# Kernel optimization log

Hardware: AMD Instinct MI355X
Metric: run time of the kernel (lower is better)

## Reference

```python
import jax, jax.numpy as jnp
import numpy as np
from functools import partial

STRIDE = 32
NUM_CLASSES = 20
CONF_THRESH = 0.01
NMS_THRESH = 0.5
H = W = 96
C = 512


def setup_inputs() -> dict:
    key = jax.random.key(0)
    ks = jax.random.split(key, 6)
    cls_feat = jax.random.normal(ks[0], (1, C, H, W), dtype=jnp.float32)
    reg_feat = jax.random.normal(ks[1], (1, C, H, W), dtype=jnp.float32)
    # small init scale so sigmoid/exp stay in a realistic range
    obj_w = jax.random.normal(ks[2], (1, C), dtype=jnp.float32) * 0.05
    cls_w = jax.random.normal(ks[3], (NUM_CLASSES, C), dtype=jnp.float32) * 0.05
    reg_w = jax.random.normal(ks[4], (4, C), dtype=jnp.float32) * 0.05
    obj_b = jnp.zeros((1,), jnp.float32)
    cls_b = jnp.zeros((NUM_CLASSES,), jnp.float32)
    reg_b = jnp.zeros((4,), jnp.float32)
    return {"cls_feat": cls_feat, "reg_feat": reg_feat,
            "obj_w": obj_w, "obj_b": obj_b,
            "cls_w": cls_w, "cls_b": cls_b,
            "reg_w": reg_w, "reg_b": reg_b}


def _decode_and_score(cls_feat, reg_feat, obj_w, obj_b, cls_w, cls_b, reg_w, reg_b):
    # 1x1 convs == per-pixel matmul; permute(0,2,3,1).flatten(1,2), take batch 0
    _, _, h, w = cls_feat.shape
    obj = jnp.einsum('bchw,oc->bhwo', cls_feat, obj_w)[0].reshape(h * w, 1) + obj_b
    cls = jnp.einsum('bchw,oc->bhwo', cls_feat, cls_w)[0].reshape(h * w, NUM_CLASSES) + cls_b
    reg = jnp.einsum('bchw,oc->bhwo', reg_feat, reg_w)[0].reshape(h * w, 4) + reg_b
    scores_all = jax.nn.sigmoid(obj) * jax.nn.sigmoid(cls)            # [N, 20]
    # decode_boxes: grid of (x, y) cell coords, stride 32
    gy, gx = jnp.meshgrid(jnp.arange(h), jnp.arange(w), indexing='ij')
    grid = jnp.stack([gx, gy], axis=-1).reshape(-1, 2).astype(jnp.float32)
    ctr = (jax.nn.sigmoid(reg[:, :2]) + grid) * STRIDE               # [N, 2]
    wh = jnp.exp(reg[:, 2:]) * STRIDE                                # [N, 2]
    bboxes = jnp.concatenate([ctr - 0.5 * wh, ctr + 0.5 * wh], axis=-1)  # x1y1x2y2
    return bboxes, scores_all


@jax.jit
def reference(cls_feat, reg_feat, obj_w, obj_b, cls_w, cls_b, reg_w, reg_b):
    bboxes, scores_all = _decode_and_score(
        cls_feat, reg_feat, obj_w, obj_b, cls_w, cls_b, reg_w, reg_b)
    n = bboxes.shape[0]
    labels = jnp.argmax(scores_all, axis=1)                          # [N]
    scores = jnp.max(scores_all, axis=1)                             # [N]
    valid = scores >= CONF_THRESH
    # sort by score descending (invalid boxes pushed last)
    order = jnp.argsort(-jnp.where(valid, scores, -jnp.inf))
    b = bboxes[order]
    lab_s = labels[order]
    valid_s = valid[order]
    x1, y1, x2, y2 = b[:, 0], b[:, 1], b[:, 2], b[:, 3]
    areas = (x2 - x1) * (y2 - y1)
    # pairwise IoU, matching the numpy nms (1e-10 clamp on w/h)
    iw = jnp.maximum(1e-10, jnp.minimum(x2[:, None], x2[None, :]) - jnp.maximum(x1[:, None], x1[None, :]))
    ih = jnp.maximum(1e-10, jnp.minimum(y2[:, None], y2[None, :]) - jnp.maximum(y1[:, None], y1[None, :]))
    inter = iw * ih
    iou = inter / (areas[:, None] + areas[None, :] - inter)
    same_cls = lab_s[:, None] == lab_s[None, :]
    supp = (iou > NMS_THRESH) & same_cls                             # [N, N] suppression graph
    idx = jnp.arange(n)
    # greedy per-class NMS in score order: box i is kept iff no earlier
    # kept box of the same class has IoU > thresh with it
    def body(i, keep):
        suppressed = jnp.any(keep & supp[:, i] & (idx < i))
        return keep.at[i].set(valid_s[i] & ~suppressed)
    keep_s = jax.lax.fori_loop(0, n, body, jnp.zeros(n, dtype=bool))
    keep = jnp.zeros(n, dtype=bool).at[order].set(keep_s)            # unsort
    return bboxes, scores, labels, keep


if __name__ == '__main__':
    out = reference(**setup_inputs())
    print([o.shape for o in out], int(out[3].sum()))
```

## Files before the change

kernel.cpp:

```cpp
#include <hip/hip_runtime.h>

#define HW 9216
#define WIDTH 96
#define NCLS 20
#define NOUT 25
#define CAP 1024
#define NW 16

#define WS_KEYS   256
#define WS_PART   164096
#define WS_MASK   7536896

__global__ __launch_bounds__(256) void gemm_stage1(
    const float* __restrict__ cls_feat, const float* __restrict__ reg_feat,
    const float* __restrict__ obj_w, const float* __restrict__ cls_w,
    const float* __restrict__ reg_w, float* __restrict__ partial,
    unsigned* __restrict__ cnt)
{
    if (blockIdx.x == 0 && threadIdx.x < 64) cnt[threadIdx.x] = 0u;

    __shared__ float wlds[64 * 28];
    const int g   = blockIdx.x & 7;
    const int pos = (blockIdx.x >> 3) * 256 + threadIdx.x;
    const int cb  = g * 64;

    for (int i = threadIdx.x; i < 64 * 25; i += 256) {
        const int o = i >> 6, k = i & 63;
        float v;
        if (o == 0)        v = obj_w[cb + k];
        else if (o < 21)   v = cls_w[(o - 1) * 512 + cb + k];
        else               v = reg_w[(o - 21) * 512 + cb + k];
        wlds[k * 28 + o] = v;
    }
    __syncthreads();

    float acc[NOUT];
#pragma unroll
    for (int o = 0; o < NOUT; ++o) acc[o] = 0.f;

    const float* cf = cls_feat + (size_t)cb * HW + pos;
    const float* rf = reg_feat + (size_t)cb * HW + pos;

#pragma unroll 8
    for (int k = 0; k < 64; ++k) {
        float f = cf[(size_t)k * HW];
        float h = rf[(size_t)k * HW];
        const float4* w = (const float4*)(wlds + k * 28);
        float4 w0 = w[0], w1 = w[1], w2 = w[2], w3 = w[3], w4v = w[4], w5 = w[5], w6 = w[6];
        acc[0]  += f * w0.x;  acc[1]  += f * w0.y;  acc[2]  += f * w0.z;  acc[3]  += f * w0.w;
        acc[4]  += f * w1.x;  acc[5]  += f * w1.y;  acc[6]  += f * w1.z;  acc[7]  += f * w1.w;
        acc[8]  += f * w2.x;  acc[9]  += f * w2.y;  acc[10] += f * w2.z;  acc[11] += f * w2.w;
        acc[12] += f * w3.x;  acc[13] += f * w3.y;  acc[14] += f * w3.z;  acc[15] += f * w3.w;
        acc[16] += f * w4v.x; acc[17] += f * w4v.y; acc[18] += f * w4v.z; acc[19] += f * w4v.w;
        acc[20] += f * w5.x;
        acc[21] += h * w5.y;  acc[22] += h * w5.z;  acc[23] += h * w5.w;  acc[24] += h * w6.x;
    }

    float* pg = partial + (size_t)g * NOUT * HW + pos;
#pragma unroll
    for (int o = 0; o < NOUT; ++o) pg[(size_t)o * HW] = acc[o];
}

__global__ __launch_bounds__(256, 1) void decode_stage2(
    const float* __restrict__ partial,
    const float* __restrict__ obj_b, const float* __restrict__ cls_b,
    const float* __restrict__ reg_b,
    float* __restrict__ out, unsigned* __restrict__ cnt,
    unsigned long long* __restrict__ keys)
{
    const int pp = blockIdx.x * 256 + threadIdx.x;

    float d[NOUT];
#pragma unroll
    for (int o = 0; o < NOUT; ++o) {
        float s = 0.f;
#pragma unroll
        for (int g = 0; g < 8; ++g)
            s += partial[((size_t)g * NOUT + o) * HW + pp];
        d[o] = s;
    }

    float obj  = d[0] + obj_b[0];
    float best = d[1] + cls_b[0];
    int   bk   = 0;
#pragma unroll
    for (int k = 1; k < NCLS; ++k) {
        float v = d[1 + k] + cls_b[k];
        if (v > best) { best = v; bk = k; }
    }
    float sobj  = 1.f / (1.f + expf(-obj));
    float scls  = 1.f / (1.f + expf(-best));
    float score = sobj * scls;

    float r0 = d[21] + reg_b[0], r1 = d[22] + reg_b[1];
    float r2 = d[23] + reg_b[2], r3 = d[24] + reg_b[3];
    float gx = (float)(pp % WIDTH), gy = (float)(pp / WIDTH);
    float cx = (1.f / (1.f + expf(-r0)) + gx) * 32.f;
    float cy = (1.f / (1.f + expf(-r1)) + gy) * 32.f;
    float bw = expf(r2) * 32.f;
    float bh = expf(r3) * 32.f;
    float hx = 0.5f * bw, hy = 0.5f * bh;

    ((float4*)out)[pp] = make_float4(cx - hx, cy - hy, cx + hx, cy + hy);
    out[HW * 4 + pp] = score;
    out[HW * 5 + pp] = (float)bk;
    out[HW * 6 + pp] = 0.f;

    if (score >= 0.01f) {
        unsigned slot = atomicAdd(&cnt[bk], 1u);
        if (slot < CAP) {
            unsigned sb = __float_as_uint(score) ^ 0xffffffffu;
            keys[bk * CAP + slot] = ((unsigned long long)sb << 32) | (unsigned)pp;
        }
    }
}

__device__ __forceinline__ unsigned long long shflxor64(unsigned long long v, int msk) {
    unsigned lo = __shfl_xor((unsigned)v, msk, 64);
    unsigned hi = __shfl_xor((unsigned)(v >> 32), msk, 64);
    return ((unsigned long long)hi << 32) | lo;
}

__global__ __launch_bounds__(1024) void sort_kernel(
    const unsigned* __restrict__ cnt, unsigned long long* __restrict__ keys)
{
    __shared__ unsigned long long a[CAP];
    const int c = blockIdx.x, i = threadIdx.x;
    unsigned m = cnt[c]; if (m > CAP) m = CAP;

    unsigned long long v = (i < (int)m) ? keys[c * CAP + i]
                                        : 0xFFFFFFFFFFFFFFFFull;

    for (int k = 2; k <= CAP; k <<= 1) {
        for (int j = k >> 1; j > 0; j >>= 1) {
            unsigned long long u;
            if (j >= 64) {
                __syncthreads();
                a[i] = v;
                __syncthreads();
                u = a[i ^ j];
            } else {
                u = shflxor64(v, j);
            }
            const bool takeSmall = (((i & k) == 0) == ((i & j) == 0));
            const bool less = v < u;
            v = (takeSmall == less) ? v : u;
        }
    }
    if (i < (int)m) keys[c * CAP + i] = v;
}

__global__ __launch_bounds__(1024) void build_kernel(
    const unsigned* __restrict__ cnt, const unsigned long long* __restrict__ keys,
    const float* __restrict__ bboxes, unsigned long long* __restrict__ mask)
{
    __shared__ float4 box[CAP];
    const int c = blockIdx.x >> 4, tile = blockIdx.x & 15;
    const int tid = threadIdx.x, wave = tid >> 6, lane = tid & 63;
    int m = (int)cnt[c]; if (m > CAP) m = CAP;
    const int rbase = tile << 6;
    if (rbase >= m) return;

    if (tid < m) {
        unsigned idx = (unsigned)(keys[c * CAP + tid] & 0xffffffffu);
        box[tid] = ((const float4*)bboxes)[idx];
    } else {
        box[tid] = make_float4(0.f, 0.f, 0.f, 0.f);
    }
    __syncthreads();

    unsigned long long* mrow = mask + (size_t)c * CAP * NW;
#pragma unroll 4
    for (int j = 0; j < 64; ++j) {
        const int row = rbase + (wave << 2) + (j >> 4);
        const int w   = j & 15;
        const float4 bi = box[row];
        const float4 bj = box[(w << 6) + lane];
        const float ai = (bi.z - bi.x) * (bi.w - bi.y);
        const float aj = (bj.z - bj.x) * (bj.w - bj.y);
        float iw = fminf(bi.z, bj.z) - fmaxf(bi.x, bj.x);
        float ih = fminf(bi.w, bj.w) - fmaxf(bi.y, bj.y);
        iw = fmaxf(iw, 1e-10f);
        ih = fmaxf(ih, 1e-10f);
        const float inter = iw * ih;
        const float iou = inter / (ai + aj - inter);
        unsigned long long word =
            __ballot((row < m) && (((w << 6) + lane) < m) && (iou > 0.5f));
        if (lane == 0) mrow[row * NW + w] = word;
    }
}

__device__ __forceinline__ unsigned long long uread64(unsigned long long v, int srclane) {
    unsigned lo = __builtin_amdgcn_readlane((unsigned)v, srclane);
    unsigned hi = __builtin_amdgcn_readlane((unsigned)(v >> 32), srclane);
    return ((unsigned long long)hi << 32) | lo;
}

__global__ __launch_bounds__(64) void sweep_kernel(
    const unsigned* __restrict__ cnt, const unsigned long long* __restrict__ keys,
    const unsigned long long* __restrict__ mask, float* __restrict__ keep)
{
    const int c = blockIdx.x, lane = threadIdx.x;
    int m = (int)cnt[c]; if (m > CAP) m = CAP;
    const int nw = (m + 63) >> 6;
    if (nw == 0) return;
    const unsigned long long* mrow = mask + (size_t)c * CAP * NW;

    const int wsel = lane & 15;
    const int rof  = lane >> 4;

    unsigned long long keyA =
        (lane < m) ? keys[c * CAP + lane] : 0ull;
    unsigned long long rowA =
        (lane < m) ? mrow[(size_t)lane * NW + 0] : 0ull;
    unsigned long long rwA[16];
#pragma unroll
    for (int j = 0; j < 16; ++j) {
        const int r = rof + (j << 2);
        rwA[j] = (r < m && wsel < nw) ? mrow[(size_t)r * NW + wsel] : 0ull;
    }

    unsigned long long remw = 0;
    for (int w = 0; w < nw; ++w) {
        const int i0 = w << 6;
        const int nb = min(64, m - i0);

        const bool more = (w + 1 < nw);
        const int  i1   = (w + 1) << 6;
        unsigned long long keyB =
            (more && i1 + lane < m) ? keys[c * CAP + i1 + lane] : 0ull;
        unsigned long long rowB =
            (more && i1 + lane < m) ? mrow[(size_t)(i1 + lane) * NW + (w + 1)] : 0ull;
        unsigned long long rwB[16];
#pragma unroll
        for (int j = 0; j < 16; ++j) {
            const int r = i1 + rof + (j << 2);
            rwB[j] = (more && r < m && wsel < nw)
                         ? mrow[(size_t)r * NW + wsel] : 0ull;
        }

        unsigned long long cur  = uread64(remw, w);
        unsigned long long kept = 0;
#pragma unroll
        for (int b = 0; b < 64; ++b) {
            unsigned long long x = uread64(rowA, b);
            unsigned long long alive = ((cur >> b) & 1ull) ^ 1ull;
            kept |= alive << b;
            cur |= x & (0ull - alive);
        }
        if (nb < 64) kept &= (1ull << nb) - 1ull;

        if (lane < nb && ((kept >> lane) & 1ull))
            keep[(unsigned)(keyA & 0xffffffffu)] = 1.0f;

        unsigned long long part = 0;
#pragma unroll
        for (int j = 0; j < 16; ++j) {
            const int b = rof + (j << 2);
            part |= rwA[j] & (0ull - ((kept >> b) & 1ull));
        }
        part |= shflxor64(part, 16);
        part |= shflxor64(part, 32);
        if (lane < NW) remw |= part;

        keyA = keyB;
        rowA = rowB;
#pragma unroll
        for (int j = 0; j < 16; ++j) rwA[j] = rwB[j];
    }
}

extern "C" void kernel_launch(void* const* d_in, const int* in_sizes, int n_in,
                              void* d_out, int out_size, void* d_ws, size_t ws_size,
                              hipStream_t stream)
{
    const float* cls_feat = (const float*)d_in[0];
    const float* reg_feat = (const float*)d_in[1];
    const float* obj_w    = (const float*)d_in[2];
    const float* obj_b    = (const float*)d_in[3];
    const float* cls_w    = (const float*)d_in[4];
    const float* cls_b    = (const float*)d_in[5];
    const float* reg_w    = (const float*)d_in[6];
    const float* reg_b    = (const float*)d_in[7];

    float* out = (float*)d_out;
    unsigned* cnt            = (unsigned*)d_ws;
    unsigned long long* keys = (unsigned long long*)((char*)d_ws + WS_KEYS);
    float* partial           = (float*)((char*)d_ws + WS_PART);
    unsigned long long* mask = (unsigned long long*)((char*)d_ws + WS_MASK);

    gemm_stage1<<<288, 256, 0, stream>>>(cls_feat, reg_feat,
                                         obj_w, cls_w, reg_w, partial, cnt);
    decode_stage2<<<HW / 256, 256, 0, stream>>>(partial, obj_b, cls_b, reg_b,
                                                out, cnt, keys);
    sort_kernel<<<NCLS, 1024, 0, stream>>>(cnt, keys);
    build_kernel<<<NCLS * 16, 1024, 0, stream>>>(cnt, keys, out, mask);
    sweep_kernel<<<NCLS, 64, 0, stream>>>(cnt, keys, mask, out + HW * 6);
}
```

Baseline: 190.9 us.

## Replace per-class bitonic sort with parallel rank-based scatter sort

Result: no change. 189.0 us (-1.0%).

```diff
diff --git a/kernel.cpp b/kernel.cpp
--- a/kernel.cpp
+++ b/kernel.cpp
@@ -10,6 +10,7 @@
 #define WS_KEYS   256
 #define WS_PART   164096
 #define WS_MASK   7536896
+#define WS_KEY2   10158336
 
 __global__ __launch_bounds__(256) void gemm_stage1(
     const float* __restrict__ cls_feat, const float* __restrict__ reg_feat,
@@ -115,39 +116,33 @@
     }
 }
 
-__device__ __forceinline__ unsigned long long shflxor64(unsigned long long v, int msk) {
-    unsigned lo = __shfl_xor((unsigned)v, msk, 64);
-    unsigned hi = __shfl_xor((unsigned)(v >> 32), msk, 64);
-    return ((unsigned long long)hi << 32) | lo;
-}
-
-__global__ __launch_bounds__(1024) void sort_kernel(
-    const unsigned* __restrict__ cnt, unsigned long long* __restrict__ keys)
-{
-    __shared__ unsigned long long a[CAP];
-    const int c = blockIdx.x, i = threadIdx.x;
-    unsigned m = cnt[c]; if (m > CAP) m = CAP;
-
-    unsigned long long v = (i < (int)m) ? keys[c * CAP + i]
-                                        : 0xFFFFFFFFFFFFFFFFull;
-
-    for (int k = 2; k <= CAP; k <<= 1) {
-        for (int j = k >> 1; j > 0; j >>= 1) {
-            unsigned long long u;
-            if (j >= 64) {
-                __syncthreads();
-                a[i] = v;
-                __syncthreads();
-                u = a[i ^ j];
-            } else {
-                u = shflxor64(v, j);
-            }
-            const bool takeSmall = (((i & k) == 0) == ((i & j) == 0));
-            const bool less = v < u;
-            v = (takeSmall == less) ? v : u;
-        }
-    }
-    if (i < (int)m) keys[c * CAP + i] = v;
+__global__ __launch_bounds__(1024) void rank_kernel(
+    const unsigned* __restrict__ cnt, const unsigned long long* __restrict__ keys,
+    unsigned long long* __restrict__ keys2)
+{
+    __shared__ unsigned long long klds[CAP];
+    const int c = blockIdx.x >> 4, tile = blockIdx.x & 15;
+    const int tid = threadIdx.x, wave = tid >> 6, lane = tid & 63;
+    int m = (int)cnt[c]; if (m > CAP) m = CAP;
+    const int rbase = tile << 6;
+    if (rbase >= m) return;
+
+    klds[tid] = (tid < m) ? keys[c * CAP + tid] : 0xFFFFFFFFFFFFFFFFull;
+    __syncthreads();
+
+#pragma unroll
+    for (int rr = 0; rr < 4; ++rr) {
+        const int row = rbase + (wave << 2) + rr;
+        const unsigned long long kr = klds[row];
+        int rank = 0;
+#pragma unroll
+        for (int w = 0; w < 16; ++w) {
+            unsigned long long kj = klds[(w << 6) + lane];
+            rank += (int)__popcll(__ballot(kj < kr));
+        }
+        if (lane == 0 && row < m)
+            keys2[c * CAP + rank] = kr;
+    }
 }
 
 __global__ __launch_bounds__(1024) void build_kernel(
@@ -190,6 +185,11 @@
     }
 }
 
+__device__ __forceinline__ unsigned long long shflxor64(unsigned long long v, int msk) {
+    unsigned lo = __shfl_xor((unsigned)v, msk, 64);
+    unsigned hi = __shfl_xor((unsigned)(v >> 32), msk, 64);
+    return ((unsigned long long)hi << 32) | lo;
+}
 __device__ __forceinline__ unsigned long long uread64(unsigned long long v, int srclane) {
     unsigned lo = __builtin_amdgcn_readlane((unsigned)v, srclane);
     unsigned hi = __builtin_amdgcn_readlane((unsigned)(v >> 32), srclane);
@@ -284,16 +284,17 @@
     const float* reg_b    = (const float*)d_in[7];
 
     float* out = (float*)d_out;
-    unsigned* cnt            = (unsigned*)d_ws;
-    unsigned long long* keys = (unsigned long long*)((char*)d_ws + WS_KEYS);
-    float* partial           = (float*)((char*)d_ws + WS_PART);
-    unsigned long long* mask = (unsigned long long*)((char*)d_ws + WS_MASK);
+    unsigned* cnt             = (unsigned*)d_ws;
+    unsigned long long* keys  = (unsigned long long*)((char*)d_ws + WS_KEYS);
+    float* partial            = (float*)((char*)d_ws + WS_PART);
+    unsigned long long* mask  = (unsigned long long*)((char*)d_ws + WS_MASK);
+    unsigned long long* keys2 = (unsigned long long*)((char*)d_ws + WS_KEY2);
 
     gemm_stage1<<<288, 256, 0, stream>>>(cls_feat, reg_feat,
                                          obj_w, cls_w, reg_w, partial, cnt);
     decode_stage2<<<HW / 256, 256, 0, stream>>>(partial, obj_b, cls_b, reg_b,
                                                 out, cnt, keys);
-    sort_kernel<<<NCLS, 1024, 0, stream>>>(cnt, keys);
-    build_kernel<<<NCLS * 16, 1024, 0, stream>>>(cnt, keys, out, mask);
-    sweep_kernel<<<NCLS, 64, 0, stream>>>(cnt, keys, mask, out + HW * 6);
-}
+    rank_kernel<<<NCLS * 16, 1024, 0, stream>>>(cnt, keys, keys2);
+    build_kernel<<<NCLS * 16, 1024, 0, stream>>>(cnt, keys2, out, mask);
+    sweep_kernel<<<NCLS, 64, 0, stream>>>(cnt, keys2, mask, out + HW * 6);
+}
```
